# Performance work log

Hardware: AMD Instinct MI355X
Metric: run time of the kernel (lower is better)

The kernel has to match this reference:

```python
import jax, jax.numpy as jnp
import numpy as np

B, T, D, H = 2, 2048, 1024, 4
DK, DV = 1024, 2048          # key_dim = d_model*expand_k, value_dim = d_model*expand_v
HK, HV = DK // H, DV // H    # 256, 512 per-head dims
LR = 16                      # gate_low_rank_dim
EPS = 1e-5
GATE_NORM = 16.0             # gate_logit_normalizer


def _xavier(k, shape, gain):
    fan_in, fan_out = shape
    lim = gain * np.sqrt(6.0 / (fan_in + fan_out))
    return jax.random.uniform(k, shape, jnp.float32, -lim, lim)


def setup_inputs() -> dict:
    key = jax.random.key(0)
    ks = jax.random.split(key, 10)
    g_qkv = 2 ** (-2.5)
    return {
        "x": jax.random.normal(ks[0], (B, T, D), jnp.float32),
        "Wq": _xavier(ks[1], (D, DK), g_qkv),
        "Wk": _xavier(ks[2], (D, DK), g_qkv),
        "Wv": _xavier(ks[3], (D, DV), g_qkv),
        "Wg": _xavier(ks[4], (D, DV), g_qkv),
        "gk_w1": _xavier(ks[5], (D, LR), g_qkv),
        "gk_w2": _xavier(ks[6], (LR, DK), g_qkv),
        "gk_b": jnp.zeros((DK,), jnp.float32),
        "Wo": _xavier(ks[7], (DV, D), 2 ** (-1)),
        "rms_w": jnp.ones((HV,), jnp.float32),
    }


def _gla_scan(q, k, v, g):
    # q,k,g: [T, hk]; v: [T, hv]. Recurrence S_t = diag(exp(g_t)) S_{t-1} + k_t v_t^T; o_t = q_t @ S_t
    S0 = jnp.zeros((q.shape[-1], v.shape[-1]), q.dtype)

    def step(S, inp):
        qt, kt, vt, gt = inp
        S = jnp.exp(gt)[:, None] * S + kt[:, None] * vt[None, :]
        return S, qt @ S

    return jax.lax.scan(step, S0, (q, k, v, g))[1]  # [T, hv]


def _forward(x, Wq, Wk, Wv, Wg, gk_w1, gk_w2, gk_b, Wo, rms_w):
    b, t = x.shape[0], x.shape[1]
    scale = HK ** -0.5
    # projections -> [b, h, t, d_head]
    q = (x @ Wq).reshape(b, t, H, HK).transpose(0, 2, 1, 3) * scale
    k = (x @ Wk).reshape(b, t, H, HK).transpose(0, 2, 1, 3)
    v = (x @ Wv).reshape(b, t, H, HV).transpose(0, 2, 1, 3)
    # low-rank forget gate, log-space, fp32
    gl = (x @ gk_w1) @ gk_w2 + gk_b
    g = (jax.nn.log_sigmoid(gl.astype(jnp.float32)) / GATE_NORM)
    g = g.reshape(b, t, H, HK).transpose(0, 2, 1, 3)
    # per-(batch, head) linear-attention recurrence
    o = jax.vmap(jax.vmap(_gla_scan))(q, k, v, g)  # [b, h, t, hv]
    # group RMSNorm over head_v_dim
    o = o.transpose(0, 2, 1, 3)  # [b, t, h, hv]
    o = o * jax.lax.rsqrt(jnp.mean(o * o, axis=-1, keepdims=True) + EPS) * rms_w
    # output gate (swish) + out projection
    o = o.reshape(b, t, DV) * jax.nn.silu(x @ Wg)
    return o @ Wo  # [b, t, d_model]


def reference(x, Wq, Wk, Wv, Wg, gk_w1, gk_w2, gk_b, Wo, rms_w):
    return _forward(x, Wq, Wk, Wv, Wg, gk_w1, gk_w2, gk_b, Wo, rms_w)
```

## Files before the change

kernel.cpp:

```cpp
#include <hip/hip_runtime.h>
#include <cstdint>
#include <cstddef>


typedef unsigned short u16;
typedef __attribute__((ext_vector_type(8))) short s8v;
typedef __attribute__((ext_vector_type(4))) float f4v;

__device__ __forceinline__ u16 f2b(float f) {
  unsigned u = __builtin_bit_cast(unsigned, f);
  unsigned r = u + 0x7FFFu + ((u >> 16) & 1u);
  return (u16)(r >> 16);
}
__device__ __forceinline__ float b2f(u16 h) {
  unsigned u = ((unsigned)h) << 16;
  return __builtin_bit_cast(float, u);
}

__device__ __forceinline__ void cp16(const void* g, void* l) {
  __builtin_amdgcn_global_load_lds(
      (const __attribute__((address_space(1))) unsigned int*)g,
      (__attribute__((address_space(3))) unsigned int*)l, 16, 0, 0);
}

__device__ __forceinline__ void stage_tile(const u16* g, int ld, u16* lds,
                                           int wv, int ln) {
  const int q = (ln & 3) ^ ((ln >> 3) & 3);
#pragma unroll
  for (int i = 0; i < 2; ++i) {
    const int c = wv * 2 + i;
    const u16* src = g + (size_t)(c * 16 + (ln >> 2)) * ld + q * 8;
    cp16(src, lds + c * 512);
  }
}

__device__ __forceinline__ void gemm_core(
    const u16* __restrict__ A, int lda, const u16* __restrict__ BT, int ldb,
    int K, u16* As, u16* Bs, f4v acc[4][4])
{
  const int tid = threadIdx.x;
  const int ln = tid & 63, wv = tid >> 6;
  const int arow = (wv >> 1) * 64 + (ln & 15);
  const int brow = (wv & 1) * 64 + (ln & 15);
  const int koff = (((ln >> 4) ^ ((ln >> 1) & 3)) * 8);
  const int nt = K >> 5;
  stage_tile(A, lda, As, wv, ln);
  stage_tile(BT, ldb, Bs, wv, ln);
  stage_tile(A + 32, lda, As + 4096, wv, ln);
  stage_tile(BT + 32, ldb, Bs + 4096, wv, ln);
  int slot = 0;
  for (int t = 0; t < nt; ++t) {
    if (t + 1 < nt) asm volatile("s_waitcnt vmcnt(4)" ::: "memory");
    else            asm volatile("s_waitcnt vmcnt(0)" ::: "memory");
    __builtin_amdgcn_s_barrier();
    __builtin_amdgcn_sched_barrier(0);
    const u16* Ab = As + slot * 4096;
    const u16* Bb = Bs + slot * 4096;
    s8v af[4], bf[4];
#pragma unroll
    for (int f = 0; f < 4; ++f)
      af[f] = *(const s8v*)(Ab + (arow + f * 16) * 32 + koff);
#pragma unroll
    for (int f = 0; f < 4; ++f)
      bf[f] = *(const s8v*)(Bb + (brow + f * 16) * 32 + koff);
#pragma unroll
    for (int mf = 0; mf < 4; ++mf)
#pragma unroll
      for (int nf = 0; nf < 4; ++nf)
        acc[mf][nf] = __builtin_amdgcn_mfma_f32_16x16x32_bf16(
            af[mf], bf[nf], acc[mf][nf], 0, 0, 0);
    __builtin_amdgcn_sched_barrier(0);
    __builtin_amdgcn_s_barrier();
    if (t + 2 < nt) {
      stage_tile(A + (t + 2) * 32, lda, As + slot * 4096, wv, ln);
      stage_tile(BT + (t + 2) * 32, ldb, Bs + slot * 4096, wv, ln);
    }
    slot ^= 1;
  }
}

__device__ __forceinline__ void frag_to_lds(u16* S, const f4v acc[4][4],
                                            int ln, int wv) {
  u16* q = S + wv * 4608;
#pragma unroll
  for (int mf = 0; mf < 4; ++mf)
#pragma unroll
    for (int nf = 0; nf < 4; ++nf)
#pragma unroll
      for (int r = 0; r < 4; ++r)
        q[(mf * 16 + ((ln >> 4) << 2) + r) * 72 + nf * 16 + (ln & 15)] =
            f2b(acc[mf][nf][r]);
}

template <typename F>
__device__ __forceinline__ void epi_loop(u16* S, const f4v acc[4][4], F f) {
  const int tid = threadIdx.x;
  frag_to_lds(S, acc, tid & 63, tid >> 6);
  __syncthreads();
#pragma unroll
  for (int p = 0; p < 8; ++p) {
    const int r = p * 16 + (tid >> 4);
    const int c0 = (tid & 15) * 8;
    const int quad = ((r >> 6) << 1) + (c0 >> 6);
    s8v vv = *(const s8v*)(S + quad * 4608 + (r & 63) * 72 + (c0 & 63));
    f(r, c0, vv);
  }
}

__global__ __launch_bounds__(256) void cast_b(const float* __restrict__ in,
                                              u16* __restrict__ out) {
  const int i = blockIdx.x * 256 + threadIdx.x;
  const float4 v = ((const float4*)in)[i];
  u16* p = out + i * 4;
  p[0] = f2b(v.x); p[1] = f2b(v.y); p[2] = f2b(v.z); p[3] = f2b(v.w);
}

__global__ __launch_bounds__(256) void wtrans_all(
    const float* __restrict__ Wq, const float* __restrict__ Wk,
    const float* __restrict__ Wv, const float* __restrict__ Wg,
    const float* __restrict__ Wo, u16* __restrict__ WTa, u16* __restrict__ WoT)
{
  __shared__ float t[32][33];
  const int id = blockIdx.x;
  const float* src; u16* dst; int R, C, local;
  if (id < 1024)      { src = Wq; dst = WTa;           R = 1024; C = 1024; local = id; }
  else if (id < 2048) { src = Wk; dst = WTa + 1048576; R = 1024; C = 1024; local = id - 1024; }
  else if (id < 4096) { src = Wv; dst = WTa + 2097152; R = 1024; C = 2048; local = id - 2048; }
  else if (id < 6144) { src = Wg; dst = WTa + 4194304; R = 1024; C = 2048; local = id - 4096; }
  else                { src = Wo; dst = WoT;           R = 2048; C = 1024; local = id - 6144; }
  const int nx = C >> 5;
  const int c0 = (local % nx) * 32, r0 = (local / nx) * 32;
  const int lx = threadIdx.x & 31, ly = threadIdx.x >> 5;
#pragma unroll
  for (int i = 0; i < 32; i += 8)
    t[ly + i][lx] = src[(size_t)(r0 + ly + i) * C + c0 + lx];
  __syncthreads();
#pragma unroll
  for (int i = 0; i < 32; i += 8)
    dst[(size_t)(c0 + ly + i) * R + r0 + lx] = f2b(t[lx][ly + i]);
}

__global__ __launch_bounds__(256) void trans_all(
    const u16* __restrict__ kt, u16* __restrict__ ktT,
    const u16* __restrict__ vr, u16* __restrict__ vT)
{
  __shared__ u16 t[32][33];
  const int id = blockIdx.x;
  const u16* in; u16* out; int R = 2048, C, z, local;
  if (id < 4096) { in = kt; out = ktT; C = 256;  z = id >> 9;  local = id & 511; }
  else { const int i2 = id - 4096; in = vr; out = vT; C = 512; z = i2 >> 10; local = i2 & 1023; }
  const int nx = C >> 5;
  const int c0 = (local % nx) * 32, r0 = (local / nx) * 32;
  const size_t boff = (size_t)z * R * C;
  const int lx = threadIdx.x & 31, ly = threadIdx.x >> 5;
#pragma unroll
  for (int i = 0; i < 32; i += 8)
    t[ly + i][lx] = in[boff + (size_t)(r0 + ly + i) * C + c0 + lx];
  __syncthreads();
#pragma unroll
  for (int i = 0; i < 32; i += 8)
    out[boff + (size_t)(c0 + ly + i) * R + r0 + lx] = t[lx][ly + i];
}

__global__ __launch_bounds__(256) void lowrank1(
    const float* __restrict__ x, const float* __restrict__ w1,
    float* __restrict__ tmp)
{
  const int idx = blockIdx.x * 256 + threadIdx.x;
  const int m = idx >> 4, i = idx & 15;
  const float* xr = x + (size_t)m * 1024;
  float acc = 0.f;
#pragma unroll 4
  for (int kk = 0; kk < 1024; kk += 4) {
    const float4 xv = *(const float4*)(xr + kk);
    acc = fmaf(xv.x, w1[(kk + 0) * 16 + i], acc);
    acc = fmaf(xv.y, w1[(kk + 1) * 16 + i], acc);
    acc = fmaf(xv.z, w1[(kk + 2) * 16 + i], acc);
    acc = fmaf(xv.w, w1[(kk + 3) * 16 + i], acc);
  }
  tmp[idx] = acc;
}

__global__ __launch_bounds__(256) void gate_cum(
    const float* __restrict__ tmp, const float* __restrict__ w2,
    const float* __restrict__ bias, u16* __restrict__ dq, u16* __restrict__ dk,
    float* __restrict__ Dc)
{
  __shared__ float ls_t[2048];
  const int b = blockIdx.y >> 4, c = blockIdx.y & 15;
  const int h = blockIdx.x;
  const int i = threadIdx.x;
  const int n = h * 256 + i;
  const int bh = b * 4 + h;
  const float* tp = tmp + ((size_t)(b * 2048 + c * 128)) * 16;
#pragma unroll
  for (int r = 0; r < 8; ++r) ls_t[r * 256 + threadIdx.x] = tp[r * 256 + threadIdx.x];
  __syncthreads();
  float w2c[16];
#pragma unroll
  for (int r = 0; r < 16; ++r) w2c[r] = w2[r * 1024 + n];
  const float bn = bias[n];
  const size_t base = ((size_t)bh * 2048 + c * 128) * 256 + i;
  float B = 0.f;
  for (int t = 0; t < 128; ++t) {
    float gl = bn;
    const float* tr = ls_t + t * 16;
#pragma unroll
    for (int r = 0; r < 16; ++r) gl = fmaf(tr[r], w2c[r], gl);
    const float ls = fminf(gl, 0.f) - log1pf(expf(-fabsf(gl)));
    B += ls * 0.0625f;
    const float eB = expf(B);
    dq[base + (size_t)t * 256] = f2b(eB);
    dk[base + (size_t)t * 256] = f2b(1.f / eB);
  }
  Dc[(bh * 16 + c) * 256 + i] = expf(B);
}

__global__ __launch_bounds__(256) void proj_all(
    const u16* __restrict__ xb, const u16* __restrict__ WT,
    const u16* __restrict__ dq, const u16* __restrict__ dk,
    u16* __restrict__ qt, u16* __restrict__ kt,
    u16* __restrict__ vr, u16* __restrict__ gpre)
{
  __shared__ __align__(16) u16 S[18432];
  u16* As = S; u16* Bs = S + 8192;
  const int id = blockIdx.x;
  const int xcd = id & 7, jb = id >> 3;
  const int m0 = (jb / 6) * 128;
  const int n0 = (xcd * 6 + (jb % 6)) * 128;
  f4v acc[4][4];
#pragma unroll
  for (int zi = 0; zi < 4; ++zi)
#pragma unroll
    for (int zj = 0; zj < 4; ++zj) acc[zi][zj] = (f4v){0.f, 0.f, 0.f, 0.f};
  gemm_core(xb + (size_t)m0 * 1024, 1024, WT + (size_t)n0 * 1024, 1024, 1024,
            As, Bs, acc);
  epi_loop(S, acc, [&](int r, int c0, s8v vv) {
    const int m = m0 + r;
    const int n = n0 + c0;
    const int bb = m >> 11;
    const int t = m & 2047;
    if (n0 < 1024) {
      const int bh = bb * 4 + (n >> 8);
      const int i = n & 255;
      const size_t off = ((size_t)bh * 2048 + t) * 256 + i;
      const s8v dv = *(const s8v*)(dq + off);
      s8v o8;
#pragma unroll
      for (int e = 0; e < 8; ++e)
        o8[e] = (short)f2b(b2f((u16)vv[e]) * 0.0625f * b2f((u16)dv[e]));
      *(s8v*)(qt + off) = o8;
    } else if (n0 < 2048) {
      const int nn = n - 1024;
      const int bh = bb * 4 + (nn >> 8);
      const int i = nn & 255;
      const size_t off = ((size_t)bh * 2048 + t) * 256 + i;
      const s8v dv = *(const s8v*)(dk + off);
      s8v o8;
#pragma unroll
      for (int e = 0; e < 8; ++e)
        o8[e] = (short)f2b(b2f((u16)vv[e]) * b2f((u16)dv[e]));
      *(s8v*)(kt + off) = o8;
    } else if (n0 < 4096) {
      const int nn = n - 2048;
      const int bh = bb * 4 + (nn >> 9);
      const int jj = nn & 511;
      *(s8v*)(vr + ((size_t)bh * 2048 + t) * 512 + jj) = vv;
    } else {
      *(s8v*)(gpre + (size_t)m * 2048 + (n - 4096)) = vv;
    }
  });
}

__global__ __launch_bounds__(256) void scan_gemms(
    const u16* __restrict__ vT, const u16* __restrict__ ktT,
    const u16* __restrict__ qt, const u16* __restrict__ kt,
    u16* __restrict__ UT, u16* __restrict__ Aw)
{
  __shared__ __align__(16) u16 S[18432];
  u16* As = S; u16* Bs = S + 8192;
  const int bhc = blockIdx.y, bh = bhc >> 4, c = bhc & 15;
  f4v acc[4][4];
#pragma unroll
  for (int zi = 0; zi < 4; ++zi)
#pragma unroll
    for (int zj = 0; zj < 4; ++zj) acc[zi][zj] = (f4v){0.f, 0.f, 0.f, 0.f};
  if (blockIdx.x < 8) {
    const int mt = blockIdx.x >> 1, nt = blockIdx.x & 1;
    gemm_core(vT + ((size_t)bh * 512 + mt * 128) * 2048 + c * 128, 2048,
              ktT + ((size_t)bh * 256 + nt * 128) * 2048 + c * 128, 2048, 128,
              As, Bs, acc);
    epi_loop(S, acc, [&](int r, int c0, s8v vv) {
      const int j = mt * 128 + r;
      const int i = nt * 128 + c0;
      *(s8v*)(UT + (((size_t)(bh * 512 + j)) * 16 + c) * 256 + i) = vv;
    });
  } else {
    const size_t base = ((size_t)bh * 2048 + c * 128) * 256;
    gemm_core(qt + base, 256, kt + base, 256, 256, As, Bs, acc);
    u16* Ap = Aw + (size_t)bhc * 16384;
    epi_loop(S, acc, [&](int r, int c0, s8v vv) {
      s8v o8;
#pragma unroll
      for (int e = 0; e < 8; ++e)
        o8[e] = (c0 + e <= r) ? vv[e] : (short)0;
      *(s8v*)(Ap + r * 128 + c0) = o8;
    });
  }
}

__global__ __launch_bounds__(256) void state_scan(
    u16* __restrict__ UT, const float* __restrict__ Dc)
{
  const int blk = blockIdx.x;
  const int bh = blk >> 9, j = blk & 511;
  const int i = threadIdx.x;
  u16* Up = UT + ((size_t)(bh * 512 + j)) * 16 * 256 + i;
  const float* Dp = Dc + bh * 16 * 256 + i;
  float Sa = 0.f;
  for (int c = 0; c < 16; ++c) {
    const float u = b2f(Up[c * 256]);
    Up[c * 256] = f2b(Sa);
    Sa = Dp[c * 256] * (Sa + u);
  }
}

__global__ __launch_bounds__(256) void intra_k(
    const u16* __restrict__ Aw, const u16* __restrict__ qt,
    const u16* __restrict__ vT, const u16* __restrict__ UT, u16* __restrict__ ob)
{
  __shared__ __align__(16) u16 S[18432];
  u16* As = S; u16* Bs = S + 8192;
  const int jt = blockIdx.x;
  const int bhc = blockIdx.y, bh = bhc >> 4, c = bhc & 15;
  f4v acc[4][4];
#pragma unroll
  for (int zi = 0; zi < 4; ++zi)
#pragma unroll
    for (int zj = 0; zj < 4; ++zj) acc[zi][zj] = (f4v){0.f, 0.f, 0.f, 0.f};
  gemm_core(Aw + (size_t)bhc * 16384, 128,
            vT + ((size_t)bh * 512 + jt * 128) * 2048 + c * 128, 2048, 128,
            As, Bs, acc);
  gemm_core(qt + ((size_t)bh * 2048 + c * 128) * 256, 256,
            UT + ((size_t)(bh * 512 + jt * 128)) * 4096 + (size_t)c * 256, 4096, 256,
            As, Bs, acc);
  const int b = bh >> 2, h = bh & 3;
  epi_loop(S, acc, [&](int r, int c0, s8v vv) {
    const int t = c * 128 + r;
    const int j = jt * 128 + c0;
    *(s8v*)(ob + ((size_t)(b * 2048 + t)) * 2048 + h * 512 + j) = vv;
  });
}

__global__ __launch_bounds__(256) void rms_silu(
    u16* __restrict__ o, const u16* __restrict__ gpre, const float* __restrict__ w)
{
  const int grp = blockIdx.x * 4 + (threadIdx.x >> 6);
  const int lane = threadIdx.x & 63;
  const size_t base = (size_t)(grp >> 2) * 2048 + (grp & 3) * 512;
  float xv[8];
  float ss = 0.f;
#pragma unroll
  for (int i = 0; i < 8; ++i) {
    xv[i] = b2f(o[base + i * 64 + lane]);
    ss = fmaf(xv[i], xv[i], ss);
  }
#pragma unroll
  for (int off = 1; off < 64; off <<= 1) ss += __shfl_xor(ss, off, 64);
  const float r = rsqrtf(ss * (1.f / 512.f) + 1e-5f);
#pragma unroll
  for (int i = 0; i < 8; ++i) {
    const int cidx = i * 64 + lane;
    const float gp = b2f(gpre[base + cidx]);
    const float sig = 1.f / (1.f + expf(-gp));
    o[base + cidx] = f2b(xv[i] * r * w[cidx] * gp * sig);
  }
}

__global__ __launch_bounds__(256) void gemm_out(
    const u16* __restrict__ ob, const u16* __restrict__ WoT,
    float* __restrict__ pout)
{
  __shared__ __align__(16) u16 S[18432];
  u16* As = S; u16* Bs = S + 8192;
  const int id = blockIdx.x;
  const int wg = (id & 7) * 64 + (id >> 3);
  const int ks = wg >> 8;
  const int tt = wg & 255;
  const int m0 = (tt & 31) * 128, n0 = (tt >> 5) * 128;
  f4v acc[4][4];
#pragma unroll
  for (int zi = 0; zi < 4; ++zi)
#pragma unroll
    for (int zj = 0; zj < 4; ++zj) acc[zi][zj] = (f4v){0.f, 0.f, 0.f, 0.f};
  gemm_core(ob + (size_t)m0 * 2048 + ks * 1024, 2048,
            WoT + (size_t)n0 * 2048 + ks * 1024, 2048, 1024, As, Bs, acc);
  const int tid = threadIdx.x;
  const int ln = tid & 63, wv = tid >> 6;
  const int wr = wv >> 1, wc = wv & 1;
  float* po = pout + (size_t)ks * 4194304;
#pragma unroll
  for (int mf = 0; mf < 4; ++mf)
#pragma unroll
    for (int nf = 0; nf < 4; ++nf)
#pragma unroll
      for (int r = 0; r < 4; ++r) {
        const int m = m0 + wr * 64 + mf * 16 + ((ln >> 4) << 2) + r;
        const int n = n0 + wc * 64 + nf * 16 + (ln & 15);
        po[(size_t)m * 1024 + n] = acc[mf][nf][r];
      }
}

__global__ __launch_bounds__(256) void reduce_out(
    const float* __restrict__ p, float* __restrict__ out)
{
  const int i = blockIdx.x * 256 + threadIdx.x;
  const float4 a = ((const float4*)p)[i];
  const float4 b = ((const float4*)(p + 4194304))[i];
  ((float4*)out)[i] = make_float4(a.x + b.x, a.y + b.y, a.z + b.z, a.w + b.w);
}

extern "C" void kernel_launch(void* const* d_in, const int* in_sizes, int n_in,
                              void* d_out, int out_size, void* d_ws, size_t ws_size,
                              hipStream_t stream) {
  const float* x    = (const float*)d_in[0];
  const float* Wq   = (const float*)d_in[1];
  const float* Wk   = (const float*)d_in[2];
  const float* Wv   = (const float*)d_in[3];
  const float* Wg   = (const float*)d_in[4];
  const float* w1   = (const float*)d_in[5];
  const float* w2   = (const float*)d_in[6];
  const float* gb   = (const float*)d_in[7];
  const float* Wo   = (const float*)d_in[8];
  const float* rmsw = (const float*)d_in[9];
  float* out = (float*)d_out;

  char* W = (char*)d_ws;
  u16*   xb   = (u16*)W;   W += (size_t)8  << 20;
  u16*   WTa  = (u16*)W;   W += (size_t)12 << 20;
  u16*   WoT  = (u16*)W;   W += (size_t)4  << 20;
  u16*   qt   = (u16*)W;   W += (size_t)8  << 20;
  u16*   kt   = (u16*)W;   W += (size_t)8  << 20;
  u16*   vr   = (u16*)W;   W += (size_t)16 << 20;
  u16*   vT   = (u16*)W;   W += (size_t)16 << 20;
  u16*   ktT  = (u16*)W;   W += (size_t)8  << 20;
  u16*   gpre = (u16*)W;   W += (size_t)16 << 20;
  float* tmp  = (float*)W; W += (size_t)256 << 10;
  float* Dc   = (float*)W; W += (size_t)128 << 10;
  u16*   dq   = (u16*)W;   W += (size_t)8  << 20;
  u16*   dk   = (u16*)W;   W += (size_t)8  << 20;
  u16*   UT   = (u16*)W;   W += (size_t)32 << 20;
  u16*   Aw   = (u16*)W;   W += (size_t)4  << 20;
  u16*   ob   = (u16*)W;   W += (size_t)16 << 20;
  float* pout = (float*)W; W += (size_t)32 << 20;

  hipLaunchKernelGGL(lowrank1, dim3(256), dim3(256), 0, stream, x, w1, tmp);
  hipLaunchKernelGGL(gate_cum, dim3(4, 32), dim3(256), 0, stream,
                     tmp, w2, gb, dq, dk, Dc);

  hipLaunchKernelGGL(cast_b, dim3(4096), dim3(256), 0, stream, x, xb);
  hipLaunchKernelGGL(wtrans_all, dim3(8192), dim3(256), 0, stream,
                     Wq, Wk, Wv, Wg, Wo, WTa, WoT);

  hipLaunchKernelGGL(proj_all, dim3(1536), dim3(256), 0, stream,
                     xb, WTa, dq, dk, qt, kt, vr, gpre);

  hipLaunchKernelGGL(trans_all, dim3(12288), dim3(256), 0, stream,
                     kt, ktT, vr, vT);

  hipLaunchKernelGGL(scan_gemms, dim3(9, 128), dim3(256), 0, stream,
                     vT, ktT, qt, kt, UT, Aw);
  hipLaunchKernelGGL(state_scan, dim3(4096), dim3(256), 0, stream, UT, Dc);
  hipLaunchKernelGGL(intra_k, dim3(4, 128), dim3(256), 0, stream, Aw, qt, vT, UT, ob);

  hipLaunchKernelGGL(rms_silu, dim3(4096), dim3(256), 0, stream, ob, gpre, rmsw);
  hipLaunchKernelGGL(gemm_out, dim3(512), dim3(256), 0, stream, ob, WoT, pout);
  hipLaunchKernelGGL(reduce_out, dim3(4096), dim3(256), 0, stream, pout, out);
}
```

Before: 277.4 us.

## Write V transposed from projection epilogue and merge cast kernels

The projection GEMM epilogue now writes V directly in transposed layout (vT) through a transposed LDS staging path, so the separate transpose pass over V and its intermediate buffer go away. The x cast and weight transpose kernels are merged into one launch. Branching in the epilogue is hoisted per block. The aim is to cut one 16MB round trip through memory and some launch overhead. The cost is extra LDS transpose work and possible bank conflicts in the V epilogue.

Result: faster. 259.0 us (-6.6%).

```diff
diff --git a/kernel.cpp b/kernel.cpp
--- a/kernel.cpp
+++ b/kernel.cpp
@@ -5,6 +5,7 @@
 
 typedef unsigned short u16;
 typedef __attribute__((ext_vector_type(8))) short s8v;
+typedef __attribute__((ext_vector_type(4))) short s4v;
 typedef __attribute__((ext_vector_type(4))) float f4v;
 
 __device__ __forceinline__ u16 f2b(float f) {
@@ -92,6 +93,23 @@
             f2b(acc[mf][nf][r]);
 }
 
+__device__ __forceinline__ void frag_to_lds_T(u16* S, const f4v acc[4][4],
+                                              int ln, int wv) {
+  const int wr = wv >> 1, wc = wv & 1;
+  u16* q = S + ((wc << 1) + wr) * 4608;
+#pragma unroll
+  for (int mf = 0; mf < 4; ++mf)
+#pragma unroll
+    for (int nf = 0; nf < 4; ++nf) {
+      const int cl = nf * 16 + (ln & 15);
+      const int rl = mf * 16 + ((ln >> 4) << 2);
+      s4v o4;
+#pragma unroll
+      for (int r = 0; r < 4; ++r) o4[r] = (short)f2b(acc[mf][nf][r]);
+      *(s4v*)(q + cl * 72 + rl) = o4;
+    }
+}
+
 template <typename F>
 __device__ __forceinline__ void epi_loop(u16* S, const f4v acc[4][4], F f) {
   const int tid = threadIdx.x;
@@ -107,27 +125,43 @@
   }
 }
 
-__global__ __launch_bounds__(256) void cast_b(const float* __restrict__ in,
-                                              u16* __restrict__ out) {
-  const int i = blockIdx.x * 256 + threadIdx.x;
-  const float4 v = ((const float4*)in)[i];
-  u16* p = out + i * 4;
-  p[0] = f2b(v.x); p[1] = f2b(v.y); p[2] = f2b(v.z); p[3] = f2b(v.w);
-}
-
-__global__ __launch_bounds__(256) void wtrans_all(
-    const float* __restrict__ Wq, const float* __restrict__ Wk,
-    const float* __restrict__ Wv, const float* __restrict__ Wg,
-    const float* __restrict__ Wo, u16* __restrict__ WTa, u16* __restrict__ WoT)
+template <typename F>
+__device__ __forceinline__ void epi_loop_T(u16* S, const f4v acc[4][4], F f) {
+  const int tid = threadIdx.x;
+  frag_to_lds_T(S, acc, tid & 63, tid >> 6);
+  __syncthreads();
+#pragma unroll
+  for (int p = 0; p < 8; ++p) {
+    const int r = p * 16 + (tid >> 4);
+    const int c0 = (tid & 15) * 8;
+    const int quad = ((r >> 6) << 1) + (c0 >> 6);
+    s8v vv = *(const s8v*)(S + quad * 4608 + (r & 63) * 72 + (c0 & 63));
+    f(r, c0, vv);
+  }
+}
+
+__global__ __launch_bounds__(256) void castw_all(
+    const float* __restrict__ x, const float* __restrict__ Wq,
+    const float* __restrict__ Wk, const float* __restrict__ Wv,
+    const float* __restrict__ Wg, const float* __restrict__ Wo,
+    u16* __restrict__ xb, u16* __restrict__ WTa, u16* __restrict__ WoT)
 {
   __shared__ float t[32][33];
   const int id = blockIdx.x;
+  if (id < 4096) {
+    const int i = id * 256 + threadIdx.x;
+    const float4 v = ((const float4*)x)[i];
+    u16* p = xb + i * 4;
+    p[0] = f2b(v.x); p[1] = f2b(v.y); p[2] = f2b(v.z); p[3] = f2b(v.w);
+    return;
+  }
+  const int wid = id - 4096;
   const float* src; u16* dst; int R, C, local;
-  if (id < 1024)      { src = Wq; dst = WTa;           R = 1024; C = 1024; local = id; }
-  else if (id < 2048) { src = Wk; dst = WTa + 1048576; R = 1024; C = 1024; local = id - 1024; }
-  else if (id < 4096) { src = Wv; dst = WTa + 2097152; R = 1024; C = 2048; local = id - 2048; }
-  else if (id < 6144) { src = Wg; dst = WTa + 4194304; R = 1024; C = 2048; local = id - 4096; }
-  else                { src = Wo; dst = WoT;           R = 2048; C = 1024; local = id - 6144; }
+  if (wid < 1024)      { src = Wq; dst = WTa;           R = 1024; C = 1024; local = wid; }
+  else if (wid < 2048) { src = Wk; dst = WTa + 1048576; R = 1024; C = 1024; local = wid - 1024; }
+  else if (wid < 4096) { src = Wv; dst = WTa + 2097152; R = 1024; C = 2048; local = wid - 2048; }
+  else if (wid < 6144) { src = Wg; dst = WTa + 4194304; R = 1024; C = 2048; local = wid - 4096; }
+  else                 { src = Wo; dst = WoT;           R = 2048; C = 1024; local = wid - 6144; }
   const int nx = C >> 5;
   const int c0 = (local % nx) * 32, r0 = (local / nx) * 32;
   const int lx = threadIdx.x & 31, ly = threadIdx.x >> 5;
@@ -140,26 +174,22 @@
     dst[(size_t)(c0 + ly + i) * R + r0 + lx] = f2b(t[lx][ly + i]);
 }
 
-__global__ __launch_bounds__(256) void trans_all(
-    const u16* __restrict__ kt, u16* __restrict__ ktT,
-    const u16* __restrict__ vr, u16* __restrict__ vT)
+__global__ __launch_bounds__(256) void trans_kt(
+    const u16* __restrict__ kt, u16* __restrict__ ktT)
 {
   __shared__ u16 t[32][33];
   const int id = blockIdx.x;
-  const u16* in; u16* out; int R = 2048, C, z, local;
-  if (id < 4096) { in = kt; out = ktT; C = 256;  z = id >> 9;  local = id & 511; }
-  else { const int i2 = id - 4096; in = vr; out = vT; C = 512; z = i2 >> 10; local = i2 & 1023; }
-  const int nx = C >> 5;
-  const int c0 = (local % nx) * 32, r0 = (local / nx) * 32;
-  const size_t boff = (size_t)z * R * C;
+  const int z = id >> 9, local = id & 511;
+  const int c0 = (local & 7) * 32, r0 = (local >> 3) * 32;
+  const size_t boff = (size_t)z * 2048 * 256;
   const int lx = threadIdx.x & 31, ly = threadIdx.x >> 5;
 #pragma unroll
   for (int i = 0; i < 32; i += 8)
-    t[ly + i][lx] = in[boff + (size_t)(r0 + ly + i) * C + c0 + lx];
+    t[ly + i][lx] = kt[boff + (size_t)(r0 + ly + i) * 256 + c0 + lx];
   __syncthreads();
 #pragma unroll
   for (int i = 0; i < 32; i += 8)
-    out[boff + (size_t)(c0 + ly + i) * R + r0 + lx] = t[lx][ly + i];
+    ktT[boff + (size_t)(c0 + ly + i) * 2048 + r0 + lx] = t[lx][ly + i];
 }
 
 __global__ __launch_bounds__(256) void lowrank1(
@@ -220,7 +250,7 @@
     const u16* __restrict__ xb, const u16* __restrict__ WT,
     const u16* __restrict__ dq, const u16* __restrict__ dk,
     u16* __restrict__ qt, u16* __restrict__ kt,
-    u16* __restrict__ vr, u16* __restrict__ gpre)
+    u16* __restrict__ vT, u16* __restrict__ gpre)
 {
   __shared__ __align__(16) u16 S[18432];
   u16* As = S; u16* Bs = S + 8192;
@@ -235,41 +265,46 @@
     for (int zj = 0; zj < 4; ++zj) acc[zi][zj] = (f4v){0.f, 0.f, 0.f, 0.f};
   gemm_core(xb + (size_t)m0 * 1024, 1024, WT + (size_t)n0 * 1024, 1024, 1024,
             As, Bs, acc);
-  epi_loop(S, acc, [&](int r, int c0, s8v vv) {
-    const int m = m0 + r;
-    const int n = n0 + c0;
-    const int bb = m >> 11;
-    const int t = m & 2047;
-    if (n0 < 1024) {
+  const int bb = m0 >> 11;
+  const int t0 = m0 & 2047;
+  if (n0 < 1024) {
+    epi_loop(S, acc, [&](int r, int c0, s8v vv) {
+      const int t = t0 + r;
+      const int n = n0 + c0;
       const int bh = bb * 4 + (n >> 8);
-      const int i = n & 255;
-      const size_t off = ((size_t)bh * 2048 + t) * 256 + i;
+      const size_t off = ((size_t)bh * 2048 + t) * 256 + (n & 255);
       const s8v dv = *(const s8v*)(dq + off);
       s8v o8;
 #pragma unroll
       for (int e = 0; e < 8; ++e)
         o8[e] = (short)f2b(b2f((u16)vv[e]) * 0.0625f * b2f((u16)dv[e]));
       *(s8v*)(qt + off) = o8;
-    } else if (n0 < 2048) {
-      const int nn = n - 1024;
+    });
+  } else if (n0 < 2048) {
+    epi_loop(S, acc, [&](int r, int c0, s8v vv) {
+      const int t = t0 + r;
+      const int nn = n0 + c0 - 1024;
       const int bh = bb * 4 + (nn >> 8);
-      const int i = nn & 255;
-      const size_t off = ((size_t)bh * 2048 + t) * 256 + i;
+      const size_t off = ((size_t)bh * 2048 + t) * 256 + (nn & 255);
       const s8v dv = *(const s8v*)(dk + off);
       s8v o8;
 #pragma unroll
       for (int e = 0; e < 8; ++e)
         o8[e] = (short)f2b(b2f((u16)vv[e]) * b2f((u16)dv[e]));
       *(s8v*)(kt + off) = o8;
-    } else if (n0 < 4096) {
-      const int nn = n - 2048;
-      const int bh = bb * 4 + (nn >> 9);
-      const int jj = nn & 511;
-      *(s8v*)(vr + ((size_t)bh * 2048 + t) * 512 + jj) = vv;
-    } else {
-      *(s8v*)(gpre + (size_t)m * 2048 + (n - 4096)) = vv;
-    }
-  });
+    });
+  } else if (n0 < 4096) {
+    const int nn0 = n0 - 2048;
+    const int bh = bb * 4 + (nn0 >> 9);
+    const int jj0 = nn0 & 511;
+    epi_loop_T(S, acc, [&](int r, int c0, s8v vv) {
+      *(s8v*)(vT + ((size_t)(bh * 512 + jj0 + r)) * 2048 + t0 + c0) = vv;
+    });
+  } else {
+    epi_loop(S, acc, [&](int r, int c0, s8v vv) {
+      *(s8v*)(gpre + (size_t)(m0 + r) * 2048 + (n0 + c0 - 4096)) = vv;
+    });
+  }
 }
 
 __global__ __launch_bounds__(256) void scan_gemms(
@@ -441,7 +476,6 @@
   u16*   WoT  = (u16*)W;   W += (size_t)4  << 20;
   u16*   qt   = (u16*)W;   W += (size_t)8  << 20;
   u16*   kt   = (u16*)W;   W += (size_t)8  << 20;
-  u16*   vr   = (u16*)W;   W += (size_t)16 << 20;
   u16*   vT   = (u16*)W;   W += (size_t)16 << 20;
   u16*   ktT  = (u16*)W;   W += (size_t)8  << 20;
   u16*   gpre = (u16*)W;   W += (size_t)16 << 20;
@@ -458,15 +492,13 @@
   hipLaunchKernelGGL(gate_cum, dim3(4, 32), dim3(256), 0, stream,
                      tmp, w2, gb, dq, dk, Dc);
 
-  hipLaunchKernelGGL(cast_b, dim3(4096), dim3(256), 0, stream, x, xb);
-  hipLaunchKernelGGL(wtrans_all, dim3(8192), dim3(256), 0, stream,
-                     Wq, Wk, Wv, Wg, Wo, WTa, WoT);
+  hipLaunchKernelGGL(castw_all, dim3(12288), dim3(256), 0, stream,
+                     x, Wq, Wk, Wv, Wg, Wo, xb, WTa, WoT);
 
   hipLaunchKernelGGL(proj_all, dim3(1536), dim3(256), 0, stream,
-                     xb, WTa, dq, dk, qt, kt, vr, gpre);
-
-  hipLaunchKernelGGL(trans_all, dim3(12288), dim3(256), 0, stream,
-                     kt, ktT, vr, vT);
+                     xb, WTa, dq, dk, qt, kt, vT, gpre);
+
+  hipLaunchKernelGGL(trans_kt, dim3(4096), dim3(256), 0, stream, kt, ktT);
 
   hipLaunchKernelGGL(scan_gemms, dim3(9, 128), dim3(256), 0, stream,
                      vT, ktT, qt, kt, UT, Aw);
```
